# Performance work log

Hardware: AMD Instinct MI355X
Metric: run time of the kernel (lower is better)

Reference implementation:

```python
import jax, jax.numpy as jnp
import numpy as np

TAU = 0.1
EPS = 1e-8


def setup_inputs() -> dict:
    key = jax.random.key(0)
    k1, k2, k3 = jax.random.split(key, 3)
    B, D = 4096, 256
    features = jax.random.normal(k1, (B, D), dtype=jnp.float32)
    pos_features = jax.random.normal(k2, (B, D), dtype=jnp.float32)
    labels = jax.random.randint(k3, (B,), 0, 64, dtype=jnp.int64)
    return {"features": features, "pos_features": pos_features, "labels": labels}


def reference(features, pos_features, labels):
    # concat image and positive features / duplicate labels
    f = jnp.concatenate([features, pos_features], axis=0)          # [N, D], N = 2B
    lab = jnp.concatenate([labels, labels], axis=0)                # [N]
    N = f.shape[0]

    # cosine similarity: mm(a, a.T) / clamp(w * w.T, 1e-8)
    w = jnp.linalg.norm(f, axis=1, keepdims=True)                  # [N, 1]
    logits = (f @ f.T) / jnp.clip(w * w.T, EPS)                    # [N, N]
    z = logits / TAU

    diag = jnp.eye(N, dtype=bool)
    neg_inf = jnp.asarray(-jnp.inf, dtype=z.dtype)

    # denominator: logsumexp over all off-diagonal entries per row
    loss_all = jnp.sum(jax.nn.logsumexp(jnp.where(diag, neg_inf, z), axis=1))

    # positives: for each row, logsumexp over same-label off-diagonal entries.
    # This vectorizes the original python loop over unique labels: the union of
    # the per-label sub-matrices (diagonal removed) is exactly this mask.
    same = (lab[:, None] == lab[None, :]) & ~diag                  # [N, N]
    loss_pos = jnp.sum(jax.nn.logsumexp(jnp.where(same, z, neg_inf), axis=1))

    return loss_all - loss_pos
```

## Files before the change

### kernel.cpp

```cpp
#include <hip/hip_runtime.h>
#include <hip/hip_bf16.h>
#include <stdint.h>

#define NROWS 8192
#define DDIM  256
#define BM    128
#define BN    128
#define BK    32
#define NTILE (NROWS / BM)
#define NTRI  (NTILE * (NTILE + 1) / 2)
#define L2E   1.44269504088896340736f

#define COL_STRIDE2 5
#define ROW_STRIDE2 18
#define ROWAP_OFF   5120
#define SMEM_BYTES  (ROWAP_OFF + 128 * ROW_STRIDE2 * 8)

typedef __attribute__((ext_vector_type(8))) short short8;
typedef __attribute__((ext_vector_type(4))) float f32x4;

typedef const __attribute__((address_space(1))) uint32_t glb_u32;
typedef __attribute__((address_space(3))) uint32_t lds_u32;

__device__ __forceinline__ void load_lds16(const unsigned short* g, unsigned short* l) {
  __builtin_amdgcn_global_load_lds((glb_u32*)g, (lds_u32*)l, 16, 0, 0);
}

__device__ __forceinline__ unsigned short f2bf(float x) {
  __hip_bfloat16 h = __float2bfloat16(x);
  return *reinterpret_cast<unsigned short*>(&h);
}

__global__ void __launch_bounds__(256)
milnce_prep(const float* __restrict__ feat, const float* __restrict__ pos,
            const int* __restrict__ labels, unsigned short* __restrict__ fb,
            float* __restrict__ inv_w, int* __restrict__ lab,
            float* __restrict__ S_all, float* __restrict__ S_pos) {
  const int wave = threadIdx.x >> 6;
  const int lane = threadIdx.x & 63;
  const int row  = blockIdx.x * 4 + wave;

  const float* src = (row < 4096) ? (feat + (size_t)row * DDIM)
                                  : (pos + (size_t)(row - 4096) * DDIM);
  float4 v = ((const float4*)src)[lane];

  ushort4 o;
  o.x = f2bf(v.x); o.y = f2bf(v.y); o.z = f2bf(v.z); o.w = f2bf(v.w);
  ((ushort4*)(fb + (size_t)row * DDIM))[lane] = o;

  float ss = v.x*v.x + v.y*v.y + v.z*v.z + v.w*v.w;
  #pragma unroll
  for (int m = 1; m < 64; m <<= 1) ss += __shfl_xor(ss, m, 64);
  if (lane == 0) inv_w[row] = 1.0f / sqrtf(ss);

  const int tid = blockIdx.x * 256 + threadIdx.x;
  if (tid < NROWS) {
    lab[tid]   = labels[tid & 4095];
    S_all[tid] = 0.0f;
    S_pos[tid] = 0.0f;
  }
}

__global__ void __launch_bounds__(256)
milnce_gemm(const unsigned short* __restrict__ fb, const float* __restrict__ inv_w,
            const int* __restrict__ lab, float* __restrict__ S_all,
            float* __restrict__ S_pos) {
  __shared__ __align__(16) char smem[SMEM_BYTES];
  unsigned short* ldsA = (unsigned short*)smem;
  unsigned short* ldsB = (unsigned short*)(smem + 8192);
  float2* colAP = (float2*)smem;
  float2* rowAP = (float2*)(smem + ROWAP_OFF);

  int t = blockIdx.x, d = 0, rem = NTILE;
  while (t >= rem) { t -= rem; ++d; --rem; }
  const int bi = t, bj = t + d;

  const int tid  = threadIdx.x;
  const int wave = tid >> 6;
  const int lane = tid & 63;
  const int quad = lane >> 4;
  const int l15  = lane & 15;
  const int wm   = wave >> 1;
  const int wn   = wave & 1;
  const int rowBase = bi * BM;
  const int colBase = bj * BN;

  f32x4 acc[4][4];
  #pragma unroll
  for (int i = 0; i < 4; ++i)
    #pragma unroll
    for (int j = 0; j < 4; ++j) acc[i][j] = (f32x4){0.f, 0.f, 0.f, 0.f};

  const int s0 = wave * 64 + lane;
  const int s1 = s0 + 256;
  const int r0 = s0 >> 2, g0 = (s0 & 3) ^ ((s0 >> 3) & 3);
  const int r1 = s1 >> 2, g1 = (s1 & 3) ^ ((s1 >> 3) & 3);
  const unsigned short* gA0 = fb + (size_t)(rowBase + r0) * DDIM + g0 * 8;
  const unsigned short* gA1 = fb + (size_t)(rowBase + r1) * DDIM + g1 * 8;
  const unsigned short* gB0 = fb + (size_t)(colBase + r0) * DDIM + g0 * 8;
  const unsigned short* gB1 = fb + (size_t)(colBase + r1) * DDIM + g1 * 8;
  unsigned short* lA0 = ldsA + (size_t)(wave * 64) * 8;
  unsigned short* lA1 = ldsA + (size_t)(wave * 64 + 256) * 8;
  unsigned short* lB0 = ldsB + (size_t)(wave * 64) * 8;
  unsigned short* lB1 = ldsB + (size_t)(wave * 64 + 256) * 8;

  const int xsl = quad ^ ((l15 >> 1) & 3);

  #pragma unroll
  for (int kt = 0; kt < DDIM / BK; ++kt) {
    const int ko = kt * BK;
    __syncthreads();
    load_lds16(gA0 + ko, lA0);
    load_lds16(gA1 + ko, lA1);
    load_lds16(gB0 + ko, lB0);
    load_lds16(gB1 + ko, lB1);
    __syncthreads();

    short8 a[4], b[4];
    #pragma unroll
    for (int mi = 0; mi < 4; ++mi)
      a[mi] = *(const short8*)&ldsA[(wm * 64 + mi * 16 + l15) * BK + xsl * 8];
    #pragma unroll
    for (int ni = 0; ni < 4; ++ni)
      b[ni] = *(const short8*)&ldsB[(wn * 64 + ni * 16 + l15) * BK + xsl * 8];

    #pragma unroll
    for (int mi = 0; mi < 4; ++mi)
      #pragma unroll
      for (int ni = 0; ni < 4; ++ni)
        acc[mi][ni] = __builtin_amdgcn_mfma_f32_16x16x32_bf16(a[mi], b[ni], acc[mi][ni], 0, 0, 0);
  }

  __syncthreads();

  const float SHIFT = 10.0f * L2E;
  float cf[4]; int cl[4], colg[4];
  #pragma unroll
  for (int ni = 0; ni < 4; ++ni) {
    colg[ni] = colBase + wn * 64 + ni * 16 + l15;
    cf[ni]   = inv_w[colg[ni]] * (10.0f * L2E);
    cl[ni]   = lab[colg[ni]];
  }

  const bool offdiag = (bi != bj);

  float2 capk[4] = {{0.f,0.f},{0.f,0.f},{0.f,0.f},{0.f,0.f}};

  if (offdiag) {
    #pragma unroll
    for (int mi = 0; mi < 4; ++mi) {
      const int rbase = wm * 64 + mi * 16 + quad * 4;
      const float4 rf4 = *(const float4*)&inv_w[rowBase + rbase];
      const int4   rl4 = *(const int4*)&lab[rowBase + rbase];
      #pragma unroll
      for (int r = 0; r < 4; ++r) {
        const float rf = (r == 0) ? rf4.x : (r == 1) ? rf4.y : (r == 2) ? rf4.z : rf4.w;
        const int   rl = (r == 0) ? rl4.x : (r == 1) ? rl4.y : (r == 2) ? rl4.z : rl4.w;
        float sx = 0.f, sy = 0.f;
        #pragma unroll
        for (int ni = 0; ni < 4; ++ni) {
          float e  = exp2f(acc[mi][ni][r] * rf * cf[ni] - SHIFT);
          float ep = (rl == cl[ni]) ? e : 0.f;
          capk[ni].x += e; capk[ni].y += ep;
          sx += e; sy += ep;
        }
        rowAP[(rbase + r) * ROW_STRIDE2 + wn * 16 + l15] = make_float2(sx, sy);
      }
    }
  } else {
    #pragma unroll
    for (int mi = 0; mi < 4; ++mi) {
      const int rbase = wm * 64 + mi * 16 + quad * 4;
      const float4 rf4 = *(const float4*)&inv_w[rowBase + rbase];
      const int4   rl4 = *(const int4*)&lab[rowBase + rbase];
      #pragma unroll
      for (int r = 0; r < 4; ++r) {
        const float rf = (r == 0) ? rf4.x : (r == 1) ? rf4.y : (r == 2) ? rf4.z : rf4.w;
        const int   rl = (r == 0) ? rl4.x : (r == 1) ? rl4.y : (r == 2) ? rl4.z : rl4.w;
        const int rowg = rowBase + rbase + r;
        #pragma unroll
        for (int ni = 0; ni < 4; ++ni) {
          float e = exp2f(acc[mi][ni][r] * rf * cf[ni] - SHIFT);
          if (rowg == colg[ni]) e = 0.f;
          float ep = (rl == cl[ni]) ? e : 0.f;
          capk[ni].x += e; capk[ni].y += ep;
        }
      }
    }
  }

  #pragma unroll
  for (int ni = 0; ni < 4; ++ni)
    colAP[(wn * 64 + ni * 16 + l15) * COL_STRIDE2 + quad] = capk[ni];

  __syncthreads();

  if (tid < 128) {
    const float2* cp = &colAP[tid * COL_STRIDE2];
    float2 c0 = cp[0], c1 = cp[1], c2 = cp[2], c3 = cp[3];
    float sx = (c0.x + c1.x) + (c2.x + c3.x);
    float sy = (c0.y + c1.y) + (c2.y + c3.y);
    atomicAdd(&S_all[colBase + tid], sx);
    atomicAdd(&S_pos[colBase + tid], sy);
  } else if (offdiag) {
    const int rr = tid - 128;
    const float2* rp = &rowAP[rr * ROW_STRIDE2];
    float sx = 0.f, sy = 0.f;
    #pragma unroll
    for (int i = 0; i < 16; ++i) { sx += rp[i].x; sy += rp[i].y; }
    atomicAdd(&S_all[rowBase + rr], sx);
    atomicAdd(&S_pos[rowBase + rr], sy);
  }
}

__global__ void __launch_bounds__(1024)
milnce_final(const float* __restrict__ S_all, const float* __restrict__ S_pos,
             float* __restrict__ out) {
  __shared__ float red[16];
  float s = 0.f;
  for (int i = threadIdx.x; i < NROWS; i += 1024)
    s += logf(S_all[i]) - logf(S_pos[i]);
  #pragma unroll
  for (int m = 1; m < 64; m <<= 1) s += __shfl_xor(s, m, 64);
  const int wave = threadIdx.x >> 6;
  if ((threadIdx.x & 63) == 0) red[wave] = s;
  __syncthreads();
  if (threadIdx.x == 0) {
    float t = 0.f;
    #pragma unroll
    for (int i = 0; i < 16; ++i) t += red[i];
    out[0] = t;
  }
}

extern "C" void kernel_launch(void* const* d_in, const int* in_sizes, int n_in,
                              void* d_out, int out_size, void* d_ws, size_t ws_size,
                              hipStream_t stream) {
  const float* feat   = (const float*)d_in[0];
  const float* pos    = (const float*)d_in[1];
  const int*   labels = (const int*)d_in[2];

  char* ws = (char*)d_ws;
  unsigned short* fb    = (unsigned short*)ws;
  float*          inv_w = (float*)(ws + 4u * 1024 * 1024);
  int*            lab   = (int*)  (ws + 4u * 1024 * 1024 + 32 * 1024);
  float*          S_all = (float*)(ws + 4u * 1024 * 1024 + 64 * 1024);
  float*          S_pos = (float*)(ws + 4u * 1024 * 1024 + 96 * 1024);
  float*          out   = (float*)d_out;

  hipLaunchKernelGGL(milnce_prep, dim3(NROWS / 4), dim3(256), 0, stream,
                     feat, pos, labels, fb, inv_w, lab, S_all, S_pos);
  hipLaunchKernelGGL(milnce_gemm, dim3(NTRI), dim3(256), 0, stream,
                     fb, inv_w, lab, S_all, S_pos);
  hipLaunchKernelGGL(milnce_final, dim3(1), dim3(1024), 0, stream,
                     S_all, S_pos, out);
}
```

Before: 107.5 us.

## Pre-normalize rows, double-buffer BK=64 GEMM loads, closed-form tile index, parallel final reduce

Rows are normalized before the bf16 cast in prep, so the GEMM epilogue no longer loads per-row and per-column inverse norms and computes each exponent with a single FMA. The GEMM K-loop moves to BK=64 with a double-buffered LDS pipeline (global_load_lds prefetch of the next slice, vmcnt waits, raw s_barrier, setprio around MFMAs), and occupancy is hinted as 2 blocks per CU. The triangular tile index is computed in closed form instead of with a loop, and the final reduction runs across 32 blocks with atomics, with prep zeroing the output. The cost is 64KB of LDS per block and atomic float summation order in the final step.

```diff
diff --git a/kernel.cpp b/kernel.cpp
--- a/kernel.cpp
+++ b/kernel.cpp
@@ -6,15 +6,16 @@
 #define DDIM  256
 #define BM    128
 #define BN    128
-#define BK    32
+#define BK    64
+#define KSTEPS (DDIM / BK)
 #define NTILE (NROWS / BM)
 #define NTRI  (NTILE * (NTILE + 1) / 2)
-#define L2E   1.44269504088896340736f
+#define SCEXP 14.4269504088896340736f
 
 #define COL_STRIDE2 5
 #define ROW_STRIDE2 18
 #define ROWAP_OFF   5120
-#define SMEM_BYTES  (ROWAP_OFF + 128 * ROW_STRIDE2 * 8)
+#define SMEM_BYTES  65536
 
 typedef __attribute__((ext_vector_type(8))) short short8;
 typedef __attribute__((ext_vector_type(4))) float f32x4;
@@ -34,8 +35,8 @@
 __global__ void __launch_bounds__(256)
 milnce_prep(const float* __restrict__ feat, const float* __restrict__ pos,
             const int* __restrict__ labels, unsigned short* __restrict__ fb,
-            float* __restrict__ inv_w, int* __restrict__ lab,
-            float* __restrict__ S_all, float* __restrict__ S_pos) {
+            int* __restrict__ lab, float* __restrict__ S_all,
+            float* __restrict__ S_pos, float* __restrict__ out) {
   const int wave = threadIdx.x >> 6;
   const int lane = threadIdx.x & 63;
   const int row  = blockIdx.x * 4 + wave;
@@ -44,14 +45,15 @@
                                   : (pos + (size_t)(row - 4096) * DDIM);
   float4 v = ((const float4*)src)[lane];
 
+  float ss = v.x*v.x + v.y*v.y + v.z*v.z + v.w*v.w;
+  #pragma unroll
+  for (int m = 1; m < 64; m <<= 1) ss += __shfl_xor(ss, m, 64);
+  const float inv = 1.0f / sqrtf(ss);
+
   ushort4 o;
-  o.x = f2bf(v.x); o.y = f2bf(v.y); o.z = f2bf(v.z); o.w = f2bf(v.w);
+  o.x = f2bf(v.x * inv); o.y = f2bf(v.y * inv);
+  o.z = f2bf(v.z * inv); o.w = f2bf(v.w * inv);
   ((ushort4*)(fb + (size_t)row * DDIM))[lane] = o;
-
-  float ss = v.x*v.x + v.y*v.y + v.z*v.z + v.w*v.w;
-  #pragma unroll
-  for (int m = 1; m < 64; m <<= 1) ss += __shfl_xor(ss, m, 64);
-  if (lane == 0) inv_w[row] = 1.0f / sqrtf(ss);
 
   const int tid = blockIdx.x * 256 + threadIdx.x;
   if (tid < NROWS) {
@@ -59,21 +61,20 @@
     S_all[tid] = 0.0f;
     S_pos[tid] = 0.0f;
   }
-}
-
-__global__ void __launch_bounds__(256)
-milnce_gemm(const unsigned short* __restrict__ fb, const float* __restrict__ inv_w,
-            const int* __restrict__ lab, float* __restrict__ S_all,
-            float* __restrict__ S_pos) {
+  if (tid == 0) out[0] = 0.0f;
+}
+
+__global__ void __launch_bounds__(256, 2)
+milnce_gemm(const unsigned short* __restrict__ fb, const int* __restrict__ lab,
+            float* __restrict__ S_all, float* __restrict__ S_pos) {
   __shared__ __align__(16) char smem[SMEM_BYTES];
-  unsigned short* ldsA = (unsigned short*)smem;
-  unsigned short* ldsB = (unsigned short*)(smem + 8192);
-  float2* colAP = (float2*)smem;
-  float2* rowAP = (float2*)(smem + ROWAP_OFF);
-
-  int t = blockIdx.x, d = 0, rem = NTILE;
-  while (t >= rem) { t -= rem; ++d; --rem; }
-  const int bi = t, bj = t + d;
+
+  int t = blockIdx.x;
+  int d = (int)((129.0f - sqrtf(16641.0f - 8.0f * (float)t)) * 0.5f);
+  while (d * (129 - d) / 2 > t) --d;
+  while ((d + 1) * (128 - d) / 2 <= t) ++d;
+  const int rem = t - d * (129 - d) / 2;
+  const int bi = rem, bj = rem + d;
 
   const int tid  = threadIdx.x;
   const int wave = tid >> 6;
@@ -91,75 +92,95 @@
     #pragma unroll
     for (int j = 0; j < 4; ++j) acc[i][j] = (f32x4){0.f, 0.f, 0.f, 0.f};
 
-  const int s0 = wave * 64 + lane;
-  const int s1 = s0 + 256;
-  const int r0 = s0 >> 2, g0 = (s0 & 3) ^ ((s0 >> 3) & 3);
-  const int r1 = s1 >> 2, g1 = (s1 & 3) ^ ((s1 >> 3) & 3);
-  const unsigned short* gA0 = fb + (size_t)(rowBase + r0) * DDIM + g0 * 8;
-  const unsigned short* gA1 = fb + (size_t)(rowBase + r1) * DDIM + g1 * 8;
-  const unsigned short* gB0 = fb + (size_t)(colBase + r0) * DDIM + g0 * 8;
-  const unsigned short* gB1 = fb + (size_t)(colBase + r1) * DDIM + g1 * 8;
-  unsigned short* lA0 = ldsA + (size_t)(wave * 64) * 8;
-  unsigned short* lA1 = ldsA + (size_t)(wave * 64 + 256) * 8;
-  unsigned short* lB0 = ldsB + (size_t)(wave * 64) * 8;
-  unsigned short* lB1 = ldsB + (size_t)(wave * 64 + 256) * 8;
-
-  const int xsl = quad ^ ((l15 >> 1) & 3);
-
-  #pragma unroll
-  for (int kt = 0; kt < DDIM / BK; ++kt) {
-    const int ko = kt * BK;
-    __syncthreads();
-    load_lds16(gA0 + ko, lA0);
-    load_lds16(gA1 + ko, lA1);
-    load_lds16(gB0 + ko, lB0);
-    load_lds16(gB1 + ko, lB1);
-    __syncthreads();
-
-    short8 a[4], b[4];
-    #pragma unroll
-    for (int mi = 0; mi < 4; ++mi)
-      a[mi] = *(const short8*)&ldsA[(wm * 64 + mi * 16 + l15) * BK + xsl * 8];
-    #pragma unroll
-    for (int ni = 0; ni < 4; ++ni)
-      b[ni] = *(const short8*)&ldsB[(wn * 64 + ni * 16 + l15) * BK + xsl * 8];
-
-    #pragma unroll
-    for (int mi = 0; mi < 4; ++mi)
+  const unsigned short* gA[4];
+  const unsigned short* gB[4];
+  #pragma unroll
+  for (int i = 0; i < 4; ++i) {
+    const int s = i * 256 + wave * 64 + lane;
+    const int r = s >> 3;
+    const int g = (s & 7) ^ (r & 7);
+    gA[i] = fb + (size_t)(rowBase + r) * DDIM + g * 8;
+    gB[i] = fb + (size_t)(colBase + r) * DDIM + g * 8;
+  }
+  unsigned short* lds = (unsigned short*)smem;
+  const int dstW = wave * 512;
+
+  #pragma unroll
+  for (int i = 0; i < 4; ++i) load_lds16(gA[i], lds + dstW + i * 2048);
+  #pragma unroll
+  for (int i = 0; i < 4; ++i) load_lds16(gB[i], lds + 8192 + dstW + i * 2048);
+
+  const int jx   = (quad ^ (l15 & 7)) * 8;
+  const int rowA = (wm * 64 + l15) * BK;
+  const int rowB = (wn * 64 + l15) * BK;
+
+  #pragma unroll
+  for (int kt = 0; kt < KSTEPS; ++kt) {
+    const int cur = kt & 1;
+    if (kt + 1 < KSTEPS) {
+      const int nxtOff = (cur ^ 1) * 16384;
+      const int ko = (kt + 1) * BK;
+      #pragma unroll
+      for (int i = 0; i < 4; ++i)
+        load_lds16(gA[i] + ko, lds + nxtOff + dstW + i * 2048);
+      #pragma unroll
+      for (int i = 0; i < 4; ++i)
+        load_lds16(gB[i] + ko, lds + nxtOff + 8192 + dstW + i * 2048);
+      asm volatile("s_waitcnt vmcnt(8)" ::: "memory");
+    } else {
+      asm volatile("s_waitcnt vmcnt(0)" ::: "memory");
+    }
+    __builtin_amdgcn_s_barrier();
+
+    const unsigned short* As = lds + cur * 16384;
+    const unsigned short* Bs = As + 8192;
+    #pragma unroll
+    for (int kk = 0; kk < 2; ++kk) {
+      short8 a[4], b[4];
+      const int jo = jx ^ (kk * 32);
+      #pragma unroll
+      for (int mi = 0; mi < 4; ++mi)
+        a[mi] = *(const short8*)&As[rowA + mi * 1024 + jo];
       #pragma unroll
       for (int ni = 0; ni < 4; ++ni)
-        acc[mi][ni] = __builtin_amdgcn_mfma_f32_16x16x32_bf16(a[mi], b[ni], acc[mi][ni], 0, 0, 0);
-  }
-
-  __syncthreads();
-
-  const float SHIFT = 10.0f * L2E;
-  float cf[4]; int cl[4], colg[4];
+        b[ni] = *(const short8*)&Bs[rowB + ni * 1024 + jo];
+      __builtin_amdgcn_s_setprio(1);
+      #pragma unroll
+      for (int mi = 0; mi < 4; ++mi)
+        #pragma unroll
+        for (int ni = 0; ni < 4; ++ni)
+          acc[mi][ni] = __builtin_amdgcn_mfma_f32_16x16x32_bf16(a[mi], b[ni], acc[mi][ni], 0, 0, 0);
+      __builtin_amdgcn_s_setprio(0);
+    }
+    asm volatile("s_waitcnt lgkmcnt(0)" ::: "memory");
+    __builtin_amdgcn_s_barrier();
+  }
+
+  float2* colAP = (float2*)smem;
+  float2* rowAP = (float2*)(smem + ROWAP_OFF);
+
+  int cl[4], colg[4];
   #pragma unroll
   for (int ni = 0; ni < 4; ++ni) {
     colg[ni] = colBase + wn * 64 + ni * 16 + l15;
-    cf[ni]   = inv_w[colg[ni]] * (10.0f * L2E);
     cl[ni]   = lab[colg[ni]];
   }
 
   const bool offdiag = (bi != bj);
-
   float2 capk[4] = {{0.f,0.f},{0.f,0.f},{0.f,0.f},{0.f,0.f}};
 
   if (offdiag) {
     #pragma unroll
     for (int mi = 0; mi < 4; ++mi) {
       const int rbase = wm * 64 + mi * 16 + quad * 4;
-      const float4 rf4 = *(const float4*)&inv_w[rowBase + rbase];
-      const int4   rl4 = *(const int4*)&lab[rowBase + rbase];
+      const int4 rl4 = *(const int4*)&lab[rowBase + rbase];
       #pragma unroll
       for (int r = 0; r < 4; ++r) {
-        const float rf = (r == 0) ? rf4.x : (r == 1) ? rf4.y : (r == 2) ? rf4.z : rf4.w;
-        const int   rl = (r == 0) ? rl4.x : (r == 1) ? rl4.y : (r == 2) ? rl4.z : rl4.w;
+        const int rl = (r == 0) ? rl4.x : (r == 1) ? rl4.y : (r == 2) ? rl4.z : rl4.w;
         float sx = 0.f, sy = 0.f;
         #pragma unroll
         for (int ni = 0; ni < 4; ++ni) {
-          float e  = exp2f(acc[mi][ni][r] * rf * cf[ni] - SHIFT);
+          float e  = exp2f(__builtin_fmaf(acc[mi][ni][r], SCEXP, -SCEXP));
           float ep = (rl == cl[ni]) ? e : 0.f;
           capk[ni].x += e; capk[ni].y += ep;
           sx += e; sy += ep;
@@ -171,16 +192,14 @@
     #pragma unroll
     for (int mi = 0; mi < 4; ++mi) {
       const int rbase = wm * 64 + mi * 16 + quad * 4;
-      const float4 rf4 = *(const float4*)&inv_w[rowBase + rbase];
-      const int4   rl4 = *(const int4*)&lab[rowBase + rbase];
+      const int4 rl4 = *(const int4*)&lab[rowBase + rbase];
       #pragma unroll
       for (int r = 0; r < 4; ++r) {
-        const float rf = (r == 0) ? rf4.x : (r == 1) ? rf4.y : (r == 2) ? rf4.z : rf4.w;
-        const int   rl = (r == 0) ? rl4.x : (r == 1) ? rl4.y : (r == 2) ? rl4.z : rl4.w;
+        const int rl = (r == 0) ? rl4.x : (r == 1) ? rl4.y : (r == 2) ? rl4.z : rl4.w;
         const int rowg = rowBase + rbase + r;
         #pragma unroll
         for (int ni = 0; ni < 4; ++ni) {
-          float e = exp2f(acc[mi][ni][r] * rf * cf[ni] - SHIFT);
+          float e = exp2f(__builtin_fmaf(acc[mi][ni][r], SCEXP, -SCEXP));
           if (rowg == colg[ni]) e = 0.f;
           float ep = (rl == cl[ni]) ? e : 0.f;
           capk[ni].x += e; capk[ni].y += ep;
@@ -198,10 +217,8 @@
   if (tid < 128) {
     const float2* cp = &colAP[tid * COL_STRIDE2];
     float2 c0 = cp[0], c1 = cp[1], c2 = cp[2], c3 = cp[3];
-    float sx = (c0.x + c1.x) + (c2.x + c3.x);
-    float sy = (c0.y + c1.y) + (c2.y + c3.y);
-    atomicAdd(&S_all[colBase + tid], sx);
-    atomicAdd(&S_pos[colBase + tid], sy);
+    atomicAdd(&S_all[colBase + tid], (c0.x + c1.x) + (c2.x + c3.x));
+    atomicAdd(&S_pos[colBase + tid], (c0.y + c1.y) + (c2.y + c3.y));
   } else if (offdiag) {
     const int rr = tid - 128;
     const float2* rp = &rowAP[rr * ROW_STRIDE2];
@@ -213,24 +230,17 @@
   }
 }
 
-__global__ void __launch_bounds__(1024)
+__global__ void __launch_bounds__(256)
 milnce_final(const float* __restrict__ S_all, const float* __restrict__ S_pos,
              float* __restrict__ out) {
-  __shared__ float red[16];
-  float s = 0.f;
-  for (int i = threadIdx.x; i < NROWS; i += 1024)
-    s += logf(S_all[i]) - logf(S_pos[i]);
+  const int i = blockIdx.x * 256 + threadIdx.x;
+  float s = logf(S_all[i]) - logf(S_pos[i]);
   #pragma unroll
   for (int m = 1; m < 64; m <<= 1) s += __shfl_xor(s, m, 64);
-  const int wave = threadIdx.x >> 6;
-  if ((threadIdx.x & 63) == 0) red[wave] = s;
+  __shared__ float red[4];
+  if ((threadIdx.x & 63) == 0) red[threadIdx.x >> 6] = s;
   __syncthreads();
-  if (threadIdx.x == 0) {
-    float t = 0.f;
-    #pragma unroll
-    for (int i = 0; i < 16; ++i) t += red[i];
-    out[0] = t;
-  }
+  if (threadIdx.x == 0) atomicAdd(out, (red[0] + red[1]) + (red[2] + red[3]));
 }
 
 extern "C" void kernel_launch(void* const* d_in, const int* in_sizes, int n_in,
@@ -242,16 +252,15 @@
 
   char* ws = (char*)d_ws;
   unsigned short* fb    = (unsigned short*)ws;
-  float*          inv_w = (float*)(ws + 4u * 1024 * 1024);
-  int*            lab   = (int*)  (ws + 4u * 1024 * 1024 + 32 * 1024);
-  float*          S_all = (float*)(ws + 4u * 1024 * 1024 + 64 * 1024);
-  float*          S_pos = (float*)(ws + 4u * 1024 * 1024 + 96 * 1024);
+  int*            lab   = (int*)  (ws + 4u * 1024 * 1024);
+  float*          S_all = (float*)(ws + 4u * 1024 * 1024 + 32 * 1024);
+  float*          S_pos = (float*)(ws + 4u * 1024 * 1024 + 64 * 1024);
   float*          out   = (float*)d_out;
 
   hipLaunchKernelGGL(milnce_prep, dim3(NROWS / 4), dim3(256), 0, stream,
-                     feat, pos, labels, fb, inv_w, lab, S_all, S_pos);
+                     feat, pos, labels, fb, lab, S_all, S_pos, out);
   hipLaunchKernelGGL(milnce_gemm, dim3(NTRI), dim3(256), 0, stream,
-                     fb, inv_w, lab, S_all, S_pos);
-  hipLaunchKernelGGL(milnce_final, dim3(1), dim3(1024), 0, stream,
+                     fb, lab, S_all, S_pos);
+  hipLaunchKernelGGL(milnce_final, dim3(32), dim3(256), 0, stream,
                      S_all, S_pos, out);
 }
```

Result: faster. 95.74 us (-10.9%).
